# Kernel tuning notes

Measured on AMD Instinct MI355X. Metric: run time of the kernel, lower is better.

Reference implementation:

```python
import jax, jax.numpy as jnp
import numpy as np

# ---- module hyperparameters (match init_kwargs) ----
SPATIAL = (32, 64)          # token grid, N = 32*64 = 2048
D_MODEL = 1024
N_HEADS = 16
HEAD_DIM = D_MODEL // N_HEADS  # 64
THETA = 10000.0
XPOS_SCALE_BASE = SPATIAL[0] * 2  # 64


def _rope_tables():
    """ND rotary (xpos) tables, lucidrains-style.
    Each spatial axis gets head_dim//ndim rotary channels; frequencies are
    interleave-repeated (r=2) to pair with rotate_half. Returns cos, sin,
    xpos scale, each [N, HEAD_DIM] float32."""
    nd = len(SPATIAL)
    dpa = HEAD_DIM // nd  # dims per axis (32)
    freqs_axes, scale_axes = [], []
    for size in SPATIAL:
        inv_freq = 1.0 / (THETA ** (np.arange(0, dpa, 2, dtype=np.float64) / dpa))
        t = np.arange(size, dtype=np.float64)
        f = np.repeat(t[:, None] * inv_freq[None, :], 2, axis=-1)        # [size, dpa]
        sbase = (np.arange(0, dpa, 2, dtype=np.float64) + 0.4 * dpa) / (1.4 * dpa)
        power = (t - size // 2) / XPOS_SCALE_BASE
        sc = np.repeat(sbase[None, :] ** power[:, None], 2, axis=-1)     # [size, dpa]
        freqs_axes.append(f)
        scale_axes.append(sc)
    # broadcast each axis table over the full grid, concat along channel dim
    def grid_concat(tabs):
        parts = []
        for i, tab in enumerate(tabs):
            shp = [1] * nd + [dpa]
            shp[i] = SPATIAL[i]
            parts.append(np.broadcast_to(tab.reshape(shp), tuple(SPATIAL) + (dpa,)))
        return np.concatenate(parts, axis=-1).reshape(-1, HEAD_DIM)  # [N, HEAD_DIM]
    freqs = grid_concat(freqs_axes)
    xscale = grid_concat(scale_axes)
    return (jnp.asarray(np.cos(freqs), jnp.float32),
            jnp.asarray(np.sin(freqs), jnp.float32),
            jnp.asarray(xscale, jnp.float32))


def _rotate_half(x):
    # pairwise rotation: (x1, x2) -> (-x2, x1), interleaved layout
    x = x.reshape(*x.shape[:-1], -1, 2)
    x1, x2 = x[..., 0], x[..., 1]
    return jnp.stack((-x2, x1), axis=-1).reshape(*x.shape[:-2], -1)


def setup_inputs() -> dict:
    key = jax.random.key(0)
    ks = jax.random.split(key, 3)
    B, N = 2, SPATIAL[0] * SPATIAL[1]
    x = jax.random.normal(ks[0], (B, N, D_MODEL), dtype=jnp.float32)
    w_qkv = jax.random.normal(ks[1], (D_MODEL, 3 * D_MODEL), dtype=jnp.float32) * 0.02
    b_qkv = jnp.zeros((3 * D_MODEL,), jnp.float32)
    w_proj = jax.random.normal(ks[2], (D_MODEL, D_MODEL), dtype=jnp.float32) * 0.02
    b_proj = jnp.zeros((D_MODEL,), jnp.float32)
    return {"x": x, "w_qkv": w_qkv, "b_qkv": b_qkv, "w_proj": w_proj, "b_proj": b_proj}


def reference(x, w_qkv, b_qkv, w_proj, b_proj):
    B, N, C = x.shape
    scale = HEAD_DIM ** -0.5
    qkv = (x @ w_qkv + b_qkv).reshape(B, N, 3, N_HEADS, HEAD_DIM)
    qkv = qkv.transpose(2, 0, 3, 1, 4)  # [3, B, H, N, D]
    q, k, v = qkv[0], qkv[1], qkv[2]
    cos, sin, xs = _rope_tables()       # [N, D], broadcast over B,H
    q = (q * cos + _rotate_half(q) * sin) * xs
    k = (k * cos + _rotate_half(k) * sin) / xs
    attn = jax.nn.softmax(jnp.einsum('bhnd,bhmd->bhnm', q, k) * scale, axis=-1)
    out = jnp.einsum('bhnm,bhmd->bhnd', attn, v)
    out = out.transpose(0, 2, 1, 3).reshape(B, N, C)
    return out @ w_proj + b_proj
```

## Files before the change

kernel.cpp:

```cpp
#include <hip/hip_runtime.h>
#include <math.h>

typedef __attribute__((ext_vector_type(8))) _Float16 f16x8;
typedef __attribute__((ext_vector_type(4))) _Float16 f16x4;
typedef __attribute__((ext_vector_type(4))) float f32x4;
typedef __attribute__((ext_vector_type(16))) float f32x16;

#define MFMAH(a, b, c) __builtin_amdgcn_mfma_f32_16x16x32_f16((a), (b), (c), 0, 0, 0)
#define MFMA32(a, b, c) __builtin_amdgcn_mfma_f32_32x32x16_f16((a), (b), (c), 0, 0, 0)

#define QSCALE 0.18033688011112042f
#define SOFF 4.328085122666891f


__device__ __forceinline__ void gl_lds16(const _Float16* g, _Float16* l) {
    __builtin_amdgcn_global_load_lds(
        (const __attribute__((address_space(1))) unsigned int*)g,
        (__attribute__((address_space(3))) unsigned int*)l, 16, 0, 0);
}

__device__ __forceinline__ unsigned pkh(float a, float b) {
    union { _Float16 h[2]; unsigned u; } x;
    x.h[0] = (_Float16)a;
    x.h[1] = (_Float16)b;
    return x.u;
}

__global__ void prep_kernel(const float* __restrict__ x, const float* __restrict__ w_qkv,
                            const float* __restrict__ w_proj, _Float16* __restrict__ xb,
                            _Float16* __restrict__ wq, _Float16* __restrict__ wp,
                            float* __restrict__ ct, float* __restrict__ st,
                            float* __restrict__ xt) {
    __shared__ float tile[32][33];
    const int b = blockIdx.x, tid = threadIdx.x;
    if (b < 4096) {
        int i = (b * 256 + tid) * 4;
        float4 v = *(const float4*)&x[i];
        f16x4 h = {(_Float16)v.x, (_Float16)v.y, (_Float16)v.z, (_Float16)v.w};
        *(f16x4*)&xb[i] = h;
    } else if (b < 4096 + 3072 + 1024) {
        int t, C;
        const float* src;
        _Float16* dst;
        if (b < 4096 + 3072) { t = b - 4096; C = 3072; src = w_qkv; dst = wq; }
        else                 { t = b - 4096 - 3072; C = 1024; src = w_proj; dst = wp; }
        const int tr = t & 31, tc = t >> 5;
        const int tx = tid & 31, ty = tid >> 5;
#pragma unroll
        for (int yy = 0; yy < 4; ++yy) {
            int r = ty + yy * 8;
            tile[r][tx] = src[(size_t)(tr * 32 + r) * C + tc * 32 + tx];
        }
        __syncthreads();
#pragma unroll
        for (int yy = 0; yy < 4; ++yy) {
            int r = ty + yy * 8;
            dst[(size_t)(tc * 32 + r) * 1024 + tr * 32 + tx] = (_Float16)tile[tx][r];
        }
    } else {
        int i = (b - 8192) * 256 + tid;
        int n = i >> 6, d = i & 63;
        int gi = n >> 6, gj = n & 63;
        int axis = d >> 5;
        int p = (d & 31) >> 1;
        float t = axis ? (float)gj : (float)gi;
        float half = axis ? 32.0f : 16.0f;
        float inv_freq = powf(10000.0f, -(float)p * (1.0f / 16.0f));
        float fr = t * inv_freq;
        float sbase = (2.0f * p + 12.8f) / 44.8f;
        float xs = powf(sbase, (t - half) * (1.0f / 64.0f));
        ct[i] = cosf(fr);
        st[i] = sinf(fr);
        xt[i] = xs;
    }
}

__global__ __launch_bounds__(256) void gemm_qkv_kernel(
    const _Float16* __restrict__ A_g, const _Float16* __restrict__ B_g,
    const float* __restrict__ bias, const float* __restrict__ ctab,
    const float* __restrict__ stab, const float* __restrict__ xtab,
    _Float16* __restrict__ qb, _Float16* __restrict__ kb, _Float16* __restrict__ vt) {
    __shared__ __align__(16) _Float16 Asm[4096];
    __shared__ __align__(16) _Float16 Bsm[4096];

    const int tid = threadIdx.x;
    const int lane = tid & 63, wave = tid >> 6;
    const int quad = lane >> 4, l16 = lane & 15;
    const int wm = wave >> 1, wn = wave & 1;
    const int m0 = blockIdx.x * 128, n0 = blockIdx.y * 128;

    f32x4 zero = {0.f, 0.f, 0.f, 0.f};
    f32x4 acc[4][4];
#pragma unroll
    for (int i = 0; i < 4; ++i)
#pragma unroll
        for (int j = 0; j < 4; ++j) acc[i][j] = zero;

    const int c1t = tid + 256;
    const int row0 = tid >> 2, s0 = tid & 3;
    const int row1 = c1t >> 2, s1 = c1t & 3;
    const int g0 = s0 ^ ((row0 >> 1) & 3);
    const int g1 = s1 ^ ((row1 >> 1) & 3);
    const _Float16* Ap0 = &A_g[(size_t)(m0 + row0) * 1024 + (g0 << 3)];
    const _Float16* Ap1 = &A_g[(size_t)(m0 + row1) * 1024 + (g1 << 3)];
    const _Float16* Bp0 = &B_g[(size_t)(n0 + row0) * 1024 + (g0 << 3)];
    const _Float16* Bp1 = &B_g[(size_t)(n0 + row1) * 1024 + (g1 << 3)];
    _Float16* La0 = &Asm[tid * 8];
    _Float16* La1 = &Asm[c1t * 8];
    _Float16* Lb0 = &Bsm[tid * 8];
    _Float16* Lb1 = &Bsm[c1t * 8];

    const int sw = (l16 >> 1) & 3;

    for (int k0 = 0; k0 < 1024; k0 += 32) {
        __syncthreads();
        gl_lds16(Ap0 + k0, La0);
        gl_lds16(Ap1 + k0, La1);
        gl_lds16(Bp0 + k0, Lb0);
        gl_lds16(Bp1 + k0, Lb1);
        __syncthreads();

        f16x8 af[4], bf[4];
#pragma unroll
        for (int i = 0; i < 4; ++i) {
            af[i] = *(const f16x8*)&Asm[(wm * 64 + i * 16 + l16) * 32 + ((quad ^ sw) << 3)];
            bf[i] = *(const f16x8*)&Bsm[(wn * 64 + i * 16 + l16) * 32 + ((quad ^ sw) << 3)];
        }
#pragma unroll
        for (int i = 0; i < 4; ++i)
#pragma unroll
            for (int j = 0; j < 4; ++j) acc[i][j] = MFMAH(af[i], bf[j], acc[i][j]);
    }

    float bj[4];
#pragma unroll
    for (int j = 0; j < 4; ++j) bj[j] = bias[n0 + wn * 64 + j * 16 + l16];

    if (n0 < 2048) {
#pragma unroll
        for (int i = 0; i < 4; ++i) {
#pragma unroll
            for (int r = 0; r < 4; ++r) {
                const int row = m0 + wm * 64 + i * 16 + quad * 4 + r;
                const int b = row >> 11, nrow = row & 2047;
#pragma unroll
                for (int j = 0; j < 4; ++j) {
                    const int col = n0 + wn * 64 + j * 16 + l16;
                    float v = acc[i][j][r] + bj[j];
                    float partner = __shfl_xor(v, 1);
                    const int hh = (col >> 6) & 15;
                    const int d = col & 63;
                    const size_t o = ((size_t)(b * 16 + hh) * 2048 + nrow) * 64 + d;
                    float rh = (d & 1) ? partner : -partner;
                    const int ti = nrow * 64 + d;
                    float rv = v * ctab[ti] + rh * stab[ti];
                    float xs = xtab[ti];
                    if (col < 1024)
                        qb[o] = (_Float16)(rv * xs * QSCALE);
                    else
                        kb[o] = (_Float16)(rv / xs);
                }
            }
        }
    } else {
#pragma unroll
        for (int i = 0; i < 4; ++i) {
            const int row = m0 + wm * 64 + i * 16 + quad * 4;
            const int b = row >> 11, nrow = row & 2047;
#pragma unroll
            for (int j = 0; j < 4; ++j) {
                const int col = n0 + wn * 64 + j * 16 + l16;
                const int hh = (col >> 6) & 15;
                const int d = col & 63;
                f16x4 pv4;
#pragma unroll
                for (int r = 0; r < 4; ++r) pv4[r] = (_Float16)(acc[i][j][r] + bj[j]);
                *(f16x4*)&vt[((size_t)(b * 16 + hh) * 64 + d) * 2048 + nrow] = pv4;
            }
        }
    }
}

__global__ __launch_bounds__(256) void gemm_proj_kernel(
    const _Float16* __restrict__ A_g, const _Float16* __restrict__ B_g,
    const float* __restrict__ bias, float* __restrict__ out) {
    __shared__ __align__(16) _Float16 Asm[4096];
    __shared__ __align__(16) _Float16 Bsm[2048];

    const int tid = threadIdx.x;
    const int lane = tid & 63, wave = tid >> 6;
    const int quad = lane >> 4, l16 = lane & 15;
    const int wm = wave >> 1, wn = wave & 1;
    const int m0 = blockIdx.x * 128, n0 = blockIdx.y * 64;

    f32x4 zero = {0.f, 0.f, 0.f, 0.f};
    f32x4 acc[4][2];
#pragma unroll
    for (int i = 0; i < 4; ++i)
#pragma unroll
        for (int j = 0; j < 2; ++j) acc[i][j] = zero;

    const int c1t = tid + 256;
    const int row0 = tid >> 2, s0 = tid & 3;
    const int row1 = c1t >> 2, s1 = c1t & 3;
    const int g0 = s0 ^ ((row0 >> 1) & 3);
    const int g1 = s1 ^ ((row1 >> 1) & 3);
    const _Float16* Ap0 = &A_g[(size_t)(m0 + row0) * 1024 + (g0 << 3)];
    const _Float16* Ap1 = &A_g[(size_t)(m0 + row1) * 1024 + (g1 << 3)];
    const _Float16* Bp0 = &B_g[(size_t)(n0 + row0) * 1024 + (g0 << 3)];
    _Float16* La0 = &Asm[tid * 8];
    _Float16* La1 = &Asm[c1t * 8];
    _Float16* Lb0 = &Bsm[tid * 8];

    const int sw = (l16 >> 1) & 3;

    for (int k0 = 0; k0 < 1024; k0 += 32) {
        __syncthreads();
        gl_lds16(Ap0 + k0, La0);
        gl_lds16(Ap1 + k0, La1);
        gl_lds16(Bp0 + k0, Lb0);
        __syncthreads();

        f16x8 af[4], bf[2];
#pragma unroll
        for (int i = 0; i < 4; ++i)
            af[i] = *(const f16x8*)&Asm[(wm * 64 + i * 16 + l16) * 32 + ((quad ^ sw) << 3)];
#pragma unroll
        for (int j = 0; j < 2; ++j)
            bf[j] = *(const f16x8*)&Bsm[(wn * 32 + j * 16 + l16) * 32 + ((quad ^ sw) << 3)];
#pragma unroll
        for (int i = 0; i < 4; ++i)
#pragma unroll
            for (int j = 0; j < 2; ++j) acc[i][j] = MFMAH(af[i], bf[j], acc[i][j]);
    }

    float bj[2];
#pragma unroll
    for (int j = 0; j < 2; ++j) bj[j] = bias[n0 + wn * 32 + j * 16 + l16];
#pragma unroll
    for (int i = 0; i < 4; ++i)
#pragma unroll
        for (int r = 0; r < 4; ++r) {
            const int row = m0 + wm * 64 + i * 16 + quad * 4 + r;
#pragma unroll
            for (int j = 0; j < 2; ++j) {
                const int col = n0 + wn * 32 + j * 16 + l16;
                out[(size_t)row * 1024 + col] = acc[i][j][r] + bj[j];
            }
        }
}

#define KLD 72

__global__ __launch_bounds__(256) void attn_kernel(
    const _Float16* __restrict__ qb, const _Float16* __restrict__ kb,
    const _Float16* __restrict__ vt, _Float16* __restrict__ ao) {
    __shared__ __align__(16) _Float16 Ksm0[64 * KLD], Ksm1[64 * KLD];
    __shared__ __align__(16) _Float16 Vsm0[64 * KLD], Vsm1[64 * KLD];

    const int tid = threadIdx.x;
    const int lane = tid & 63, wave = tid >> 6;
    const int l32 = lane & 31, hi = lane >> 5, hi8 = hi << 3;
    const int bh = blockIdx.x & 31, qt = blockIdx.x >> 5;
    const size_t base = (size_t)bh * 2048 * 64;
    const int qrow0 = qt * 128 + wave * 32;

    f16x8 qf[4];
#pragma unroll
    for (int dc = 0; dc < 4; ++dc)
        qf[dc] = *(const f16x8*)&qb[base + (size_t)(qrow0 + l32) * 64 + dc * 16 + hi8];

    f32x16 moff16, zero16;
#pragma unroll
    for (int e = 0; e < 16; ++e) { moff16[e] = -SOFF; zero16[e] = 0.f; }
    f32x16 o0 = zero16, o1 = zero16;
    float lsum = 0.f;

    const int kr0 = tid >> 3, ko0 = (tid & 7) << 3;
    const int kr1 = kr0 + 32;
    f16x8 pk0, pk1, pv0, pv1;
    auto gload = [&](int kt) {
        pk0 = *(const f16x8*)&kb[base + (size_t)(kt + kr0) * 64 + ko0];
        pk1 = *(const f16x8*)&kb[base + (size_t)(kt + kr1) * 64 + ko0];
        pv0 = *(const f16x8*)&vt[((size_t)bh * 64 + kr0) * 2048 + kt + ko0];
        pv1 = *(const f16x8*)&vt[((size_t)bh * 64 + kr1) * 2048 + kt + ko0];
    };
    auto stage = [&](_Float16* Ks, _Float16* Vs) {
        *(f16x8*)&Ks[kr0 * KLD + ko0] = pk0;
        *(f16x8*)&Ks[kr1 * KLD + ko0] = pk1;
        *(f16x8*)&Vs[kr0 * KLD + ko0] = pv0;
        *(f16x8*)&Vs[kr1 * KLD + ko0] = pv1;
    };

    auto compute = [&](const _Float16* Ks, const _Float16* Vs) {
        f32x16 s0 = moff16, s1 = moff16;
#pragma unroll
        for (int dc = 0; dc < 4; ++dc) {
            f16x8 kf0 = *(const f16x8*)&Ks[l32 * KLD + dc * 16 + hi8];
            f16x8 kf1 = *(const f16x8*)&Ks[(32 + l32) * KLD + dc * 16 + hi8];
            s0 = MFMA32(kf0, qf[dc], s0);
            s1 = MFMA32(kf1, qf[dc], s1);
        }
        float p0[16], p1[16];
#pragma unroll
        for (int e = 0; e < 16; ++e) {
            p0[e] = __builtin_amdgcn_exp2f(s0[e]);
            lsum += p0[e];
        }
#pragma unroll
        for (int e = 0; e < 16; ++e) {
            p1[e] = __builtin_amdgcn_exp2f(s1[e]);
            lsum += p1[e];
        }
#pragma unroll
        for (int c = 0; c < 4; ++c) {
            const float* ps = (c < 2) ? p0 : p1;
            const int bo = (c & 1) * 8;
            unsigned lo0 = pkh(ps[bo + 0], ps[bo + 1]);
            unsigned lo1 = pkh(ps[bo + 2], ps[bo + 3]);
            unsigned hi0 = pkh(ps[bo + 4], ps[bo + 5]);
            unsigned hi1 = pkh(ps[bo + 6], ps[bo + 7]);
            unsigned send0 = hi ? lo0 : hi0;
            unsigned send1 = hi ? lo1 : hi1;
            unsigned r0 = (unsigned)__shfl_xor((int)send0, 32);
            unsigned r1 = (unsigned)__shfl_xor((int)send1, 32);
            union { unsigned w[4]; f16x8 v; } pf;
            pf.w[0] = hi ? r0 : lo0;
            pf.w[1] = hi ? r1 : lo1;
            pf.w[2] = hi ? hi0 : r0;
            pf.w[3] = hi ? hi1 : r1;
            f16x8 vf0 = *(const f16x8*)&Vs[l32 * KLD + c * 16 + hi8];
            f16x8 vf1 = *(const f16x8*)&Vs[(32 + l32) * KLD + c * 16 + hi8];
            o0 = MFMA32(pf.v, vf0, o0);
            o1 = MFMA32(pf.v, vf1, o1);
        }
    };

    gload(0);
    stage(Ksm0, Vsm0);
    gload(64);
    __syncthreads();

    for (int it = 0; it < 32; it += 2) {
        stage(Ksm1, Vsm1);
        if (it + 2 < 32) gload((it + 2) * 64);
        compute(Ksm0, Vsm0);
        __syncthreads();
        if (it + 2 < 32) stage(Ksm0, Vsm0);
        if (it + 3 < 32) gload((it + 3) * 64);
        compute(Ksm1, Vsm1);
        __syncthreads();
    }

    float vsum = lsum + __shfl_xor(lsum, 32);
    float vinv = 1.0f / vsum;
    float linv[16];
#pragma unroll
    for (int r = 0; r < 16; ++r)
        linv[r] = __shfl(vinv, (r & 3) + 8 * (r >> 2) + 4 * hi);

    const int b = bh >> 4, hh = bh & 15;
#pragma unroll
    for (int r = 0; r < 16; ++r) {
        const int qrow = qrow0 + (r & 3) + 8 * (r >> 2) + 4 * hi;
        const size_t oi = ((size_t)(b * 2048 + qrow)) * 1024 + hh * 64 + l32;
        ao[oi] = (_Float16)(o0[r] * linv[r]);
        ao[oi + 32] = (_Float16)(o1[r] * linv[r]);
    }
}

extern "C" void kernel_launch(void* const* d_in, const int* in_sizes, int n_in,
                              void* d_out, int out_size, void* d_ws, size_t ws_size,
                              hipStream_t stream) {
    const float* x = (const float*)d_in[0];
    const float* w_qkv = (const float*)d_in[1];
    const float* b_qkv = (const float*)d_in[2];
    const float* w_proj = (const float*)d_in[3];
    const float* b_proj = (const float*)d_in[4];
    float* out = (float*)d_out;

    char* ws = (char*)d_ws;
    size_t off = 0;
    auto take = [&](size_t bytes) { char* p = ws + off; off += bytes; return p; };
    _Float16* xbuf   = (_Float16*)take(8388608);
    _Float16* wqkvT  = (_Float16*)take(6291456);
    _Float16* wprojT = (_Float16*)take(2097152);
    _Float16* qbuf   = (_Float16*)take(8388608);
    _Float16* kbuf   = (_Float16*)take(8388608);
    _Float16* vtbuf  = (_Float16*)take(8388608);
    float* ctab      = (float*)take(524288);
    float* stab      = (float*)take(524288);
    float* xtab      = (float*)take(524288);
    _Float16* ao = xbuf;

    prep_kernel<<<8704, 256, 0, stream>>>(x, w_qkv, w_proj, xbuf, wqkvT, wprojT,
                                          ctab, stab, xtab);
    gemm_qkv_kernel<<<dim3(32, 24), 256, 0, stream>>>(xbuf, wqkvT, b_qkv,
                                                      ctab, stab, xtab, qbuf, kbuf, vtbuf);
    attn_kernel<<<512, 256, 0, stream>>>(qbuf, kbuf, vtbuf, ao);
    gemm_proj_kernel<<<dim3(32, 16), 256, 0, stream>>>(ao, wprojT, b_proj, out);
}
```

Measured before the change: 198.2 us.

## Split attention KV sequence across two wave groups within each block

```diff
diff --git a/kernel.cpp b/kernel.cpp
--- a/kernel.cpp
+++ b/kernel.cpp
@@ -252,18 +252,24 @@
 
 #define KLD 72
 
-__global__ __launch_bounds__(256) void attn_kernel(
+__global__ __launch_bounds__(512) void attn_kernel(
     const _Float16* __restrict__ qb, const _Float16* __restrict__ kb,
     const _Float16* __restrict__ vt, _Float16* __restrict__ ao) {
-    __shared__ __align__(16) _Float16 Ksm0[64 * KLD], Ksm1[64 * KLD];
-    __shared__ __align__(16) _Float16 Vsm0[64 * KLD], Vsm1[64 * KLD];
+    __shared__ __align__(16) _Float16 smem[8 * 64 * KLD];
 
     const int tid = threadIdx.x;
     const int lane = tid & 63, wave = tid >> 6;
+    const int w4 = wave & 3, wgrp = wave >> 2;
     const int l32 = lane & 31, hi = lane >> 5, hi8 = hi << 3;
     const int bh = blockIdx.x & 31, qt = blockIdx.x >> 5;
     const size_t base = (size_t)bh * 2048 * 64;
-    const int qrow0 = qt * 128 + wave * 32;
+    const int qrow0 = qt * 128 + w4 * 32;
+    const int kbase = wgrp << 10;
+
+    _Float16* K0 = &smem[(wgrp * 2 + 0) * 64 * KLD];
+    _Float16* K1 = &smem[(wgrp * 2 + 1) * 64 * KLD];
+    _Float16* V0 = &smem[(4 + wgrp * 2 + 0) * 64 * KLD];
+    _Float16* V1 = &smem[(4 + wgrp * 2 + 1) * 64 * KLD];
 
     f16x8 qf[4];
 #pragma unroll
@@ -276,7 +282,8 @@
     f32x16 o0 = zero16, o1 = zero16;
     float lsum = 0.f;
 
-    const int kr0 = tid >> 3, ko0 = (tid & 7) << 3;
+    const int t256 = tid & 255;
+    const int kr0 = t256 >> 3, ko0 = (t256 & 7) << 3;
     const int kr1 = kr0 + 32;
     f16x8 pk0, pk1, pv0, pv1;
     auto gload = [&](int kt) {
@@ -336,36 +343,52 @@
         }
     };
 
-    gload(0);
-    stage(Ksm0, Vsm0);
-    gload(64);
+    gload(kbase);
+    stage(K0, V0);
+    gload(kbase + 64);
     __syncthreads();
 
-    for (int it = 0; it < 32; it += 2) {
-        stage(Ksm1, Vsm1);
-        if (it + 2 < 32) gload((it + 2) * 64);
-        compute(Ksm0, Vsm0);
-        __syncthreads();
-        if (it + 2 < 32) stage(Ksm0, Vsm0);
-        if (it + 3 < 32) gload((it + 3) * 64);
-        compute(Ksm1, Vsm1);
+    for (int it = 0; it < 16; it += 2) {
+        stage(K1, V1);
+        if (it + 2 < 16) gload(kbase + (it + 2) * 64);
+        compute(K0, V0);
+        __syncthreads();
+        if (it + 2 < 16) stage(K0, V0);
+        if (it + 3 < 16) gload(kbase + (it + 3) * 64);
+        compute(K1, V1);
         __syncthreads();
     }
 
     float vsum = lsum + __shfl_xor(lsum, 32);
-    float vinv = 1.0f / vsum;
-    float linv[16];
-#pragma unroll
-    for (int r = 0; r < 16; ++r)
-        linv[r] = __shfl(vinv, (r & 3) + 8 * (r >> 2) + 4 * hi);
-
-    const int b = bh >> 4, hh = bh & 15;
-#pragma unroll
-    for (int r = 0; r < 16; ++r) {
-        const int qrow = qrow0 + (r & 3) + 8 * (r >> 2) + 4 * hi;
-        const size_t oi = ((size_t)(b * 2048 + qrow)) * 1024 + hh * 64 + l32;
-        ao[oi] = (_Float16)(o0[r] * linv[r]);
-        ao[oi + 32] = (_Float16)(o1[r] * linv[r]);
+
+    float* cb = (float*)smem;
+    if (wgrp == 1) {
+        float* p = &cb[(w4 * 64 + lane) * 33];
+#pragma unroll
+        for (int r = 0; r < 16; ++r) { p[r] = o0[r]; p[16 + r] = o1[r]; }
+        p[32] = vsum;
+    }
+    __syncthreads();
+    if (wgrp == 0) {
+        const float* p = &cb[(w4 * 64 + lane) * 33];
+#pragma unroll
+        for (int r = 0; r < 16; ++r) { o0[r] += p[r]; o1[r] += p[16 + r]; }
+        vsum += p[32];
+
+        float vinv = 1.0f / vsum;
+        float linv[16];
+#pragma unroll
+        for (int r = 0; r < 16; ++r)
+            linv[r] = __shfl(vinv, (r & 3) + 8 * (r >> 2) + 4 * hi);
+
+        const int b = bh >> 4, hh = bh & 15;
+#pragma unroll
+        for (int r = 0; r < 16; ++r) {
+            const int qrow = qrow0 + (r & 3) + 8 * (r >> 2) + 4 * hi;
+            const size_t oi = ((size_t)(b * 2048 + qrow)) * 1024 + hh * 64 + l32;
+            ao[oi] = (_Float16)(o0[r] * linv[r]);
+            ao[oi + 32] = (_Float16)(o1[r] * linv[r]);
+        }
     }
 }
 
@@ -397,6 +420,6 @@
                                           ctab, stab, xtab);
     gemm_qkv_kernel<<<dim3(32, 24), 256, 0, stream>>>(xbuf, wqkvT, b_qkv,
                                                       ctab, stab, xtab, qbuf, kbuf, vtbuf);
-    attn_kernel<<<512, 256, 0, stream>>>(qbuf, kbuf, vtbuf, ao);
+    attn_kernel<<<512, 512, 0, stream>>>(qbuf, kbuf, vtbuf, ao);
     gemm_proj_kernel<<<dim3(32, 16), 256, 0, stream>>>(ao, wprojT, b_proj, out);
 }
```

Result: no change. 197.8 us (-0.2%).
